# Optimization experiments

Measured on AMD Instinct MI355X. Metric: run time of the kernel, lower is better.

Reference implementation:

```python
import jax, jax.numpy as jnp
import numpy as np

H, DK, DV = 16, 64, 64
DECAY = 0.99
WRITE_STRENGTH = 1.0


def setup_inputs() -> dict:
    key = jax.random.key(0)
    ks = jax.random.split(key, 7)
    B, S, D = 4, 4096, 2048
    sd = 1.0 / np.sqrt(D)
    return {
        "hidden": jax.random.normal(ks[0], (B, S, D), jnp.float32),
        "memory": jax.random.normal(ks[1], (H, DK, DV), jnp.float32) * 0.02,
        "Wk": jax.random.normal(ks[2], (H * DK, D), jnp.float32) * sd,
        "Wv": jax.random.normal(ks[3], (H * DV, D), jnp.float32) * sd,
        "Wq": jax.random.normal(ks[4], (H * DK, D), jnp.float32) * sd,
        "Wg": jax.random.normal(ks[5], (D, D), jnp.float32) * sd,
        "Wo": jax.random.normal(ks[6], (D, H * DV), jnp.float32) * (1.0 / np.sqrt(H * DV)),
    }


def reference(hidden, memory, Wk, Wv, Wq, Wg, Wo):
    B, S, D = hidden.shape
    # projections (Linear, bias=False): x @ W^T
    k = (hidden @ Wk.T).reshape(B, S, H, DK)
    v = (hidden @ Wv.T).reshape(B, S, H, DV)
    q = (hidden @ Wq.T).reshape(B, S, H, DK)
    # read with pre-update memory: r = q^T M
    readout = jnp.einsum('bshk,hkv->bshv', q, memory).reshape(B, S, H * DV)
    # output gate: h' = h + sigmoid(Wg h) * (Wo r)
    gate = jax.nn.sigmoid(hidden @ Wg.T)
    out = hidden + gate * (readout @ Wo.T)
    # decaying outer-product write: M' = lambda*M + rho * sum_i k_i v_i^T
    new_memory = DECAY * memory + WRITE_STRENGTH * jnp.einsum('bshk,bshv->hkv', k, v)
    return out, new_memory
```

## Files before the change

kernel.cpp:

```cpp
#include <hip/hip_runtime.h>
#include <hip/hip_bf16.h>

typedef __attribute__((ext_vector_type(4))) float f32x4;
typedef __bf16 bf16x8 __attribute__((ext_vector_type(8)));
typedef __bf16 bf16x4 __attribute__((ext_vector_type(4)));
typedef int int4v __attribute__((ext_vector_type(4)));

#define TOKENS 16384
#define DIM    2048
#define NKVQ   3072

__device__ __forceinline__ void gload_lds16(const void* g, void* l) {
  __builtin_amdgcn_global_load_lds((const __attribute__((address_space(1))) void*)g,
                                   (__attribute__((address_space(3))) void*)l, 16, 0, 0);
}

__global__ void cast8_kernel(const float* __restrict__ src, __bf16* __restrict__ dst, int n8) {
  int i = blockIdx.x * blockDim.x + threadIdx.x;
  if (i >= n8) return;
  const float4* s = (const float4*)src;
  float4 a = s[2 * i], b = s[2 * i + 1];
  bf16x8 o;
  o[0] = (__bf16)a.x; o[1] = (__bf16)a.y; o[2] = (__bf16)a.z; o[3] = (__bf16)a.w;
  o[4] = (__bf16)b.x; o[5] = (__bf16)b.y; o[6] = (__bf16)b.z; o[7] = (__bf16)b.w;
  ((bf16x8*)dst)[i] = o;
}

__global__ void castWg_inter_kernel(const float* __restrict__ Wg, __bf16* __restrict__ W1) {
  int i = blockIdx.x * blockDim.x + threadIdx.x;
  int g = i >> 8, c8 = (i & 255) * 8;
  const float4* s = (const float4*)(Wg + (size_t)g * DIM + c8);
  float4 a = s[0], b = s[1];
  bf16x8 o;
  o[0] = (__bf16)a.x; o[1] = (__bf16)a.y; o[2] = (__bf16)a.z; o[3] = (__bf16)a.w;
  o[4] = (__bf16)b.x; o[5] = (__bf16)b.y; o[6] = (__bf16)b.z; o[7] = (__bf16)b.w;
  int r = 32 * (g >> 4) + (g & 15);
  *(bf16x8*)(W1 + (size_t)r * DIM + c8) = o;
}

__global__ void __launch_bounds__(256)
transWq_kernel(const float* __restrict__ Wq, __bf16* __restrict__ WqT) {
  __shared__ __bf16 Ts[64][68];
  const int ti = blockIdx.x >> 5, di = blockIdx.x & 31;
  const int h0 = ti << 6, d0 = di << 6;
  const int t = threadIdx.x, r0 = t >> 4, c4 = t & 15;
  #pragma unroll
  for (int i = 0; i < 4; ++i) {
    int row = r0 + i * 16;
    float4 v = *(const float4*)(Wq + (size_t)(h0 + row) * DIM + d0 + c4 * 4);
    Ts[row][c4 * 4 + 0] = (__bf16)v.x; Ts[row][c4 * 4 + 1] = (__bf16)v.y;
    Ts[row][c4 * 4 + 2] = (__bf16)v.z; Ts[row][c4 * 4 + 3] = (__bf16)v.w;
  }
  __syncthreads();
  const int d = t >> 2, sq = t & 3;
  #pragma unroll
  for (int g = 0; g < 2; ++g) {
    bf16x8 o;
    #pragma unroll
    for (int k = 0; k < 8; ++k) o[k] = Ts[sq * 16 + g * 8 + k][d];
    *(bf16x8*)(WqT + (size_t)(d0 + d) * 1024 + h0 + sq * 16 + g * 8) = o;
  }
}

__global__ void weff_kernel(const float* __restrict__ Wo, const float* __restrict__ mem,
                            __bf16* __restrict__ Weff) {
  int idx = blockIdx.x * blockDim.x + threadIdx.x;
  int d = idx >> 10, hk = idx & 1023, h = hk >> 6;
  const float* wo = Wo + d * 1024 + h * 64;
  const float* mm = mem + hk * 64;
  float s = 0.f;
  #pragma unroll 8
  for (int v = 0; v < 64; ++v) s += wo[v] * mm[v];
  Weff[idx] = (__bf16)s;
}

__device__ __forceinline__ void gemm256_core(
    const __bf16* __restrict__ A, int lda,
    const __bf16* __restrict__ B, int ldb,
    int m0, int n0, int nt, char* sm, f32x4 acc[8][4]) {

  const int tid = threadIdx.x, lane = tid & 63, wid = tid >> 6;
  const int wr = wid >> 2, wc = wid & 3;
  const int lrow = lane & 15, kc = lane >> 4;

  int offA[8], offB[4];
  #pragma unroll
  for (int m = 0; m < 8; ++m) {
    int u = (wr * 128 + m * 16 + lrow) * 4 + kc;
    offA[m] = (u ^ ((u >> 3) & 7)) << 4;
  }
  #pragma unroll
  for (int n = 0; n < 4; ++n) {
    int u = (wc * 64 + n * 16 + lrow) * 4 + kc;
    offB[n] = ((u ^ ((u >> 3) & 7)) << 4) + 16384;
  }

  const __bf16* pSA[2]; const __bf16* pSB[2];
  #pragma unroll
  for (int s = 0; s < 2; ++s) {
    int U = s * 512 + tid;
    int u = U ^ ((U >> 3) & 7);
    pSA[s] = A + (size_t)(m0 + (u >> 2)) * lda + (u & 3) * 8;
    pSB[s] = B + (size_t)(n0 + (u >> 2)) * ldb + (u & 3) * 8;
  }

  bf16x8 bvS0[4], bvS1[4];

#define BARX() asm volatile("s_barrier" ::: "memory")
#define VM4()  asm volatile("s_waitcnt vmcnt(4)" ::: "memory")
#define VM0()  asm volatile("s_waitcnt vmcnt(0)" ::: "memory")
#define NOVM
#define NOSTAGE
#define STAGE(bb, tt) do { \
    char* sA = sm + (bb) * 32768 + tid * 16; \
    gload_lds16(pSA[0] + (tt) * 32, sA); \
    gload_lds16(pSA[1] + (tt) * 32, sA + 8192); \
    gload_lds16(pSB[0] + (tt) * 32, sA + 16384); \
    gload_lds16(pSB[1] + (tt) * 32, sA + 24576); } while (0)

#define PH(bufC, bufN, C, N, STG, WT) do { \
    const char* bC = sm + (bufC) * 32768; \
    const char* bN = sm + (bufN) * 32768; \
    bf16x8 av[8]; \
    _Pragma("unroll") for (int m = 0; m < 8; ++m) av[m] = *(const bf16x8*)(bC + offA[m]); \
    _Pragma("unroll") for (int n = 0; n < 4; ++n) bvS##N[n] = *(const bf16x8*)(bN + offB[n]); \
    STG; \
    __builtin_amdgcn_s_setprio(1); \
    _Pragma("unroll") for (int m = 0; m < 8; ++m) \
      _Pragma("unroll") for (int n = 0; n < 4; ++n) \
        acc[m][n] = __builtin_amdgcn_mfma_f32_16x16x32_bf16(av[m], bvS##C[n], acc[m][n], 0, 0, 0); \
    __builtin_amdgcn_s_setprio(0); \
    WT; BARX(); } while (0)

#define PHF(bufC, C) do { \
    const char* bC = sm + (bufC) * 32768; \
    bf16x8 av[8]; \
    _Pragma("unroll") for (int m = 0; m < 8; ++m) av[m] = *(const bf16x8*)(bC + offA[m]); \
    __builtin_amdgcn_s_setprio(1); \
    _Pragma("unroll") for (int m = 0; m < 8; ++m) \
      _Pragma("unroll") for (int n = 0; n < 4; ++n) \
        acc[m][n] = __builtin_amdgcn_mfma_f32_16x16x32_bf16(av[m], bvS##C[n], acc[m][n], 0, 0, 0); \
    __builtin_amdgcn_s_setprio(0); } while (0)

  STAGE(0, 0); STAGE(1, 1); STAGE(2, 2);
  VM4(); BARX();
  #pragma unroll
  for (int n = 0; n < 4; ++n) bvS0[n] = *(const bf16x8*)(sm + offB[n]);

  for (int i = 0, e = (nt - 4) >> 2; i < e; ++i) {
    const int t = i << 2;
    PH(0, 1, 0, 1, STAGE(3, t + 3), VM4());
    PH(1, 2, 1, 0, STAGE(0, t + 4), VM4());
    PH(2, 3, 0, 1, STAGE(1, t + 5), VM4());
    PH(3, 0, 1, 0, STAGE(2, t + 6), VM4());
  }
  PH(0, 1, 0, 1, STAGE(3, nt - 1), VM4());
  PH(1, 2, 1, 0, NOSTAGE, VM0());
  PH(2, 3, 0, 1, NOSTAGE, NOVM);
  PHF(3, 1);
#undef PH
#undef PHF
#undef STAGE
#undef BARX
#undef VM4
#undef VM0
#undef NOVM
#undef NOSTAGE
}

__global__ void __launch_bounds__(512, 1)
w2_kernel(const __bf16* __restrict__ Weff, const __bf16* __restrict__ WqT,
          __bf16* __restrict__ W1) {
  __shared__ __attribute__((aligned(16))) char smem[131072];
  const int bm = blockIdx.x >> 3, bn = blockIdx.x & 7;
  const int m0 = bm * 256, n0 = bn * 256;
  f32x4 acc[8][4] = {};
  gemm256_core(Weff, 1024, WqT, 1024, m0, n0, 32, smem, acc);

  const int tid = threadIdx.x, wid = tid >> 6, lane = tid & 63;
  const int wr = wid >> 2, wc = wid & 3;
  const int crow = (lane >> 4) << 2, ccol = lane & 15;
  #pragma unroll
  for (int f = 0; f < 8; ++f) {
    int base16 = (m0 + wr * 128) >> 4;
    #pragma unroll
    for (int n = 0; n < 4; ++n) {
      int col = n0 + wc * 64 + n * 16 + ccol;
      #pragma unroll
      for (int j = 0; j < 4; ++j) {
        int r = 32 * (base16 + f) + 16 + crow + j;
        W1[(size_t)r * DIM + col] = (__bf16)acc[f][n][j];
      }
    }
  }
}

__global__ void __launch_bounds__(512, 1)
gemm_main_kernel(const __bf16* __restrict__ Xb, const __bf16* __restrict__ W1,
                 const float* __restrict__ hidden, float* __restrict__ out) {
  __shared__ __attribute__((aligned(16))) char smem[131072];
  const int x = blockIdx.x & 7;
  const int l = blockIdx.x >> 3;
  const int bm = x * 8 + (l & 7);
  const int bn = l >> 3;
  const int m0 = bm * 256, n0 = bn * 256;
  f32x4 acc[8][4] = {};
  gemm256_core(Xb, DIM, W1, DIM, m0, n0, 64, smem, acc);

  const int tid = threadIdx.x, wid = tid >> 6, lane = tid & 63;
  const int wr = wid >> 2, wc = wid & 3;
  const int crow = (lane >> 4) << 2, ccol = lane & 15;
  #pragma unroll
  for (int f = 0; f < 8; ++f) {
    int row = m0 + wr * 128 + f * 16 + crow;
    #pragma unroll
    for (int np = 0; np < 2; ++np) {
      int col = (n0 >> 1) + wc * 32 + np * 16 + ccol;
      #pragma unroll
      for (int j = 0; j < 4; ++j) {
        size_t idx = (size_t)(row + j) * DIM + col;
        float gv = 1.0f / (1.0f + __expf(-acc[f][2 * np][j]));
        out[idx] = hidden[idx] + gv * acc[f][2 * np + 1][j];
      }
    }
  }
}

__global__ void __launch_bounds__(512, 1)
gemm_kv_kernel(const __bf16* __restrict__ Xb, const __bf16* __restrict__ Wkv,
               __bf16* __restrict__ Yb) {
  __shared__ __attribute__((aligned(16))) char smem[131072];
  const int x = blockIdx.x & 7;
  const int l = blockIdx.x >> 3;
  const int bm = x * 8 + (l & 7);
  const int bn = l >> 3;
  const int m0 = bm * 256, n0 = bn * 256;
  f32x4 acc[8][4] = {};
  gemm256_core(Xb, DIM, Wkv, DIM, m0, n0, 64, smem, acc);

  __syncthreads();
  const int tid = threadIdx.x, wid = tid >> 6, lane = tid & 63;
  const int wr = wid >> 2, wc = wid & 3;
  const int crow = (lane >> 4) << 2, ccol = lane & 15;
  #pragma unroll
  for (int f = 0; f < 8; ++f)
    #pragma unroll
    for (int n = 0; n < 4; ++n)
      #pragma unroll
      for (int j = 0; j < 4; ++j) {
        int r = wr * 128 + f * 16 + crow + j;
        int c = wc * 64 + n * 16 + ccol;
        *(__bf16*)(smem + r * 512 + ((c * 2) ^ ((r & 7) << 4))) = (__bf16)acc[f][n][j];
      }
  __syncthreads();
  const int rsub = tid >> 5, ch = tid & 31;
  #pragma unroll
  for (int p = 0; p < 16; ++p) {
    int r = p * 16 + rsub;
    bf16x8 v = *(const bf16x8*)(smem + r * 512 + ((ch * 16) ^ ((r & 7) << 4)));
    __builtin_nontemporal_store(__builtin_bit_cast(int4v, v),
        (int4v*)(Yb + (size_t)(m0 + r) * NKVQ + n0 + ch * 8));
  }
}

__global__ void __launch_bounds__(256)
mem_update_kernel(const __bf16* __restrict__ Y, float* __restrict__ part) {
  const int h = blockIdx.x & 15, sp = blockIdx.x >> 4;
  __shared__ __attribute__((aligned(16))) __bf16 KT[64 * 32];
  __shared__ __attribute__((aligned(16))) __bf16 VT[64 * 32];
  const int tid = threadIdx.x, wid = tid >> 6, lane = tid & 63;
  const int lrow = lane & 15, lk = (lane >> 4) * 8;
  const __bf16* Kbase = Y + (size_t)sp * 1024 * NKVQ + h * 64;
  const __bf16* Vbase = Kbase + 1024;
  f32x4 acc[4] = {};
  const int t = tid >> 3, c8 = (tid & 7) * 8;
  for (int t0 = 0; t0 < 1024; t0 += 32) {
    __syncthreads();
    bf16x8 kv = *(const bf16x8*)(Kbase + (size_t)(t0 + t) * NKVQ + c8);
    bf16x8 vv = *(const bf16x8*)(Vbase + (size_t)(t0 + t) * NKVQ + c8);
    #pragma unroll
    for (int j = 0; j < 8; ++j) {
      KT[(c8 + j) * 32 + t] = kv[j];
      VT[(c8 + j) * 32 + t] = vv[j];
    }
    __syncthreads();
    bf16x8 af = *(const bf16x8*)(KT + (wid * 16 + lrow) * 32 + lk);
    #pragma unroll
    for (int n = 0; n < 4; ++n) {
      bf16x8 bf_ = *(const bf16x8*)(VT + (n * 16 + lrow) * 32 + lk);
      acc[n] = __builtin_amdgcn_mfma_f32_16x16x32_bf16(af, bf_, acc[n], 0, 0, 0);
    }
  }
  float* pp = part + ((size_t)sp * 16 + h) * 4096;
  const int crow = wid * 16 + (lane >> 4) * 4, ccol = lane & 15;
  #pragma unroll
  for (int n = 0; n < 4; ++n)
    #pragma unroll
    for (int r = 0; r < 4; ++r)
      pp[(crow + r) * 64 + n * 16 + ccol] = acc[n][r];
}

__global__ void mem_reduce_kernel(const float* __restrict__ part, const float* __restrict__ mem,
                                  float* __restrict__ out) {
  int i = blockIdx.x * blockDim.x + threadIdx.x;
  float s = 0.99f * mem[i];
  #pragma unroll
  for (int sp = 0; sp < 16; ++sp) s += part[sp * 65536 + i];
  out[i] = s;
}

extern "C" void kernel_launch(void* const* d_in, const int* in_sizes, int n_in,
                              void* d_out, int out_size, void* d_ws, size_t ws_size,
                              hipStream_t stream) {
  const float* hidden = (const float*)d_in[0];
  const float* memory = (const float*)d_in[1];
  const float* Wk = (const float*)d_in[2];
  const float* Wv = (const float*)d_in[3];
  const float* Wq = (const float*)d_in[4];
  const float* Wg = (const float*)d_in[5];
  const float* Wo = (const float*)d_in[6];
  float* out = (float*)d_out;
  float* mem_out = out + (size_t)TOKENS * DIM;

  char* ws = (char*)d_ws;
  __bf16* Xb   = (__bf16*)(ws);
  __bf16* W1   = (__bf16*)(ws + 67108864);
  __bf16* Wkv  = (__bf16*)(ws + 83886080);
  __bf16* Weff = (__bf16*)(ws + 92274688);
  __bf16* WqT  = (__bf16*)(ws + 96468992);
  __bf16* Yb   = (__bf16*)(ws + 100663296);
  float*  part = (float*)(ws + 201326592);

  cast8_kernel<<<16384, 256, 0, stream>>>(hidden, Xb, 4194304);
  castWg_inter_kernel<<<2048, 256, 0, stream>>>(Wg, W1);
  cast8_kernel<<<1024, 256, 0, stream>>>(Wk, Wkv, 262144);
  cast8_kernel<<<1024, 256, 0, stream>>>(Wv, Wkv + 2097152, 262144);
  weff_kernel<<<8192, 256, 0, stream>>>(Wo, memory, Weff);
  transWq_kernel<<<512, 256, 0, stream>>>(Wq, WqT);

  w2_kernel<<<64, 512, 0, stream>>>(Weff, WqT, W1);

  gemm_main_kernel<<<1024, 512, 0, stream>>>(Xb, W1, hidden, out);
  gemm_kv_kernel<<<512, 512, 0, stream>>>(Xb, Wkv, Yb);

  mem_update_kernel<<<256, 256, 0, stream>>>(Yb, part);
  mem_reduce_kernel<<<256, 256, 0, stream>>>(part, memory, mem_out);
}
```

Measured before the change: 597.5 us.

## Split-K the W2 weight-folding GEMM and merge weight cast kernels

New measurement: 615.1 us. 1.03x slower.

```diff
diff --git a/kernel.cpp b/kernel.cpp
--- a/kernel.cpp
+++ b/kernel.cpp
@@ -26,16 +26,36 @@
   ((bf16x8*)dst)[i] = o;
 }
 
-__global__ void castWg_inter_kernel(const float* __restrict__ Wg, __bf16* __restrict__ W1) {
+__global__ void prep_weights_kernel(const float* __restrict__ Wg, const float* __restrict__ Wk,
+                                    const float* __restrict__ Wv, __bf16* __restrict__ W1,
+                                    __bf16* __restrict__ Wkv) {
   int i = blockIdx.x * blockDim.x + threadIdx.x;
-  int g = i >> 8, c8 = (i & 255) * 8;
-  const float4* s = (const float4*)(Wg + (size_t)g * DIM + c8);
-  float4 a = s[0], b = s[1];
-  bf16x8 o;
-  o[0] = (__bf16)a.x; o[1] = (__bf16)a.y; o[2] = (__bf16)a.z; o[3] = (__bf16)a.w;
-  o[4] = (__bf16)b.x; o[5] = (__bf16)b.y; o[6] = (__bf16)b.z; o[7] = (__bf16)b.w;
-  int r = 32 * (g >> 4) + (g & 15);
-  *(bf16x8*)(W1 + (size_t)r * DIM + c8) = o;
+  if (i < 524288) {
+    int g = i >> 8, c8 = (i & 255) * 8;
+    const float4* s = (const float4*)(Wg + (size_t)g * DIM + c8);
+    float4 a = s[0], b = s[1];
+    bf16x8 o;
+    o[0] = (__bf16)a.x; o[1] = (__bf16)a.y; o[2] = (__bf16)a.z; o[3] = (__bf16)a.w;
+    o[4] = (__bf16)b.x; o[5] = (__bf16)b.y; o[6] = (__bf16)b.z; o[7] = (__bf16)b.w;
+    int r = 32 * (g >> 4) + (g & 15);
+    *(bf16x8*)(W1 + (size_t)r * DIM + c8) = o;
+  } else if (i < 786432) {
+    int j = i - 524288;
+    const float4* s = (const float4*)Wk + 2 * j;
+    float4 a = s[0], b = s[1];
+    bf16x8 o;
+    o[0] = (__bf16)a.x; o[1] = (__bf16)a.y; o[2] = (__bf16)a.z; o[3] = (__bf16)a.w;
+    o[4] = (__bf16)b.x; o[5] = (__bf16)b.y; o[6] = (__bf16)b.z; o[7] = (__bf16)b.w;
+    ((bf16x8*)Wkv)[j] = o;
+  } else {
+    int k = i - 786432;
+    const float4* s = (const float4*)Wv + 2 * k;
+    float4 a = s[0], b = s[1];
+    bf16x8 o;
+    o[0] = (__bf16)a.x; o[1] = (__bf16)a.y; o[2] = (__bf16)a.z; o[3] = (__bf16)a.w;
+    o[4] = (__bf16)b.x; o[5] = (__bf16)b.y; o[6] = (__bf16)b.z; o[7] = (__bf16)b.w;
+    ((bf16x8*)(Wkv + 2097152))[k] = o;
+  }
 }
 
 __global__ void __launch_bounds__(256)
@@ -169,30 +189,44 @@
 }
 
 __global__ void __launch_bounds__(512, 1)
-w2_kernel(const __bf16* __restrict__ Weff, const __bf16* __restrict__ WqT,
-          __bf16* __restrict__ W1) {
+w2split_kernel(const __bf16* __restrict__ Weff, const __bf16* __restrict__ WqT,
+               float* __restrict__ W2part) {
   __shared__ __attribute__((aligned(16))) char smem[131072];
-  const int bm = blockIdx.x >> 3, bn = blockIdx.x & 7;
+  const int ks = blockIdx.x >> 6, rr = blockIdx.x & 63;
+  const int bm = rr >> 3, bn = rr & 7;
   const int m0 = bm * 256, n0 = bn * 256;
   f32x4 acc[8][4] = {};
-  gemm256_core(Weff, 1024, WqT, 1024, m0, n0, 32, smem, acc);
-
+  gemm256_core(Weff + ks * 256, 1024, WqT + ks * 256, 1024, m0, n0, 8, smem, acc);
+
+  float* P = W2part + (size_t)ks * 4194304;
   const int tid = threadIdx.x, wid = tid >> 6, lane = tid & 63;
   const int wr = wid >> 2, wc = wid & 3;
   const int crow = (lane >> 4) << 2, ccol = lane & 15;
   #pragma unroll
   for (int f = 0; f < 8; ++f) {
-    int base16 = (m0 + wr * 128) >> 4;
+    int row = m0 + wr * 128 + f * 16 + crow;
     #pragma unroll
     for (int n = 0; n < 4; ++n) {
       int col = n0 + wc * 64 + n * 16 + ccol;
       #pragma unroll
-      for (int j = 0; j < 4; ++j) {
-        int r = 32 * (base16 + f) + 16 + crow + j;
-        W1[(size_t)r * DIM + col] = (__bf16)acc[f][n][j];
-      }
+      for (int j = 0; j < 4; ++j)
+        P[(size_t)(row + j) * 2048 + col] = acc[f][n][j];
     }
   }
+}
+
+__global__ void w2reduce_kernel(const float* __restrict__ W2part, __bf16* __restrict__ W1) {
+  int i4 = blockIdx.x * blockDim.x + threadIdx.x;
+  float4 s = ((const float4*)W2part)[i4];
+  #pragma unroll
+  for (int k = 1; k < 4; ++k) {
+    float4 p = ((const float4*)(W2part + (size_t)k * 4194304))[i4];
+    s.x += p.x; s.y += p.y; s.z += p.z; s.w += p.w;
+  }
+  int d = i4 >> 9, e4 = i4 & 511;
+  int r = 32 * (d >> 4) + 16 + (d & 15);
+  bf16x4 o; o[0] = (__bf16)s.x; o[1] = (__bf16)s.y; o[2] = (__bf16)s.z; o[3] = (__bf16)s.w;
+  *(bf16x4*)(W1 + (size_t)r * DIM + e4 * 4) = o;
 }
 
 __global__ void __launch_bounds__(512, 1)
@@ -329,16 +363,16 @@
   __bf16* Weff = (__bf16*)(ws + 92274688);
   __bf16* WqT  = (__bf16*)(ws + 96468992);
   __bf16* Yb   = (__bf16*)(ws + 100663296);
+  float*  W2part = (float*)(ws + 100663296);
   float*  part = (float*)(ws + 201326592);
 
   cast8_kernel<<<16384, 256, 0, stream>>>(hidden, Xb, 4194304);
-  castWg_inter_kernel<<<2048, 256, 0, stream>>>(Wg, W1);
-  cast8_kernel<<<1024, 256, 0, stream>>>(Wk, Wkv, 262144);
-  cast8_kernel<<<1024, 256, 0, stream>>>(Wv, Wkv + 2097152, 262144);
+  prep_weights_kernel<<<4096, 256, 0, stream>>>(Wg, Wk, Wv, W1, Wkv);
   weff_kernel<<<8192, 256, 0, stream>>>(Wo, memory, Weff);
   transWq_kernel<<<512, 256, 0, stream>>>(Wq, WqT);
 
-  w2_kernel<<<64, 512, 0, stream>>>(Weff, WqT, W1);
+  w2split_kernel<<<256, 512, 0, stream>>>(Weff, WqT, W2part);
+  w2reduce_kernel<<<4096, 256, 0, stream>>>(W2part, W1);
 
   gemm_main_kernel<<<1024, 512, 0, stream>>>(Xb, W1, hidden, out);
   gemm_kv_kernel<<<512, 512, 0, stream>>>(Xb, Wkv, Yb);
```
